# Performance work log

Measured on AMD Instinct MI355X. Metric: run time of the kernel, lower is better.

## Reference

```python
import jax, jax.numpy as jnp
import numpy as np

B, N, T = 2, 207, 864
L = 12           # patch_size
D = 96           # embed_dim
EPS = 1e-8
TAU = 1.0


def setup_inputs() -> dict:
    key = jax.random.key(0)
    k1, k2, k3, k4, k5 = jax.random.split(key, 5)
    return {
        "long_term_history": jax.random.normal(k1, (B, N, 1, T), dtype=jnp.float32),
        "adj_mx": jax.random.uniform(k2, (N, N), dtype=jnp.float32),
        "uniform_noise": jax.random.uniform(k3, (N, N), dtype=jnp.float32),
        "conv_weight": jax.random.normal(k4, (D, N, L), dtype=jnp.float32) * 0.02,
        "conv_bias": jax.random.normal(k5, (D,), dtype=jnp.float32) * 0.02,
        "k": 10,
    }


def _sample_k_neighbor_soft(adj_mx, uniform_noise, k):
    n = adj_mx.shape[0]
    logits = jnp.log(jax.nn.relu(adj_mx) + EPS)
    gumbel = -jnp.log(-jnp.log(uniform_noise + EPS))
    soft = jax.nn.softmax((logits + gumbel) / TAU, axis=1)          # [N, N]
    _, topk_idx = jax.lax.top_k(soft, k)                             # [N, k]
    hard = jnp.zeros_like(soft).at[jnp.arange(n)[:, None], topk_idx].set(1.0)
    return soft * hard                                               # [N, N]


def reference(long_term_history, adj_mx, uniform_noise, conv_weight, conv_bias, k):
    b, n, _, t = long_term_history.shape
    p = t // L
    mask = _sample_k_neighbor_soft(adj_mx, uniform_noise, k)         # [N, N]
    # expanded_history[b,i,j,t] = x[b,i,0,t]; neighbors = mask[i,j] * x[b,i,0,t]
    x = long_term_history[:, :, 0, :]                                # [B, N, T]
    neighbors = mask[None, :, :, None] * x[:, :, None, :]            # [B, N, N, T] (dense blow-up, as in source)
    xp = neighbors.reshape(b, n, n, p, L)                            # split T -> P patches of length L
    # Conv2d(N -> D, kernel (L,1), stride (L,1)) == contraction over (neighbor channel j, in-patch l)
    out = jnp.einsum('bijpl,djl->bidp', xp, conv_weight) + conv_bias[None, None, :, None]
    return out                                                       # [B, N, D, P]
```

## Files before the change

### kernel.cpp

```cpp
#include <hip/hip_runtime.h>
#include <math.h>

#define NN 207
#define BB 2
#define TT 864
#define LL 12
#define DD 96
#define PP 72
#define EPSF 1e-8f

__global__ __launch_bounds__(256) void stpe_fused_kernel(
    const float* __restrict__ x,
    const float* __restrict__ adj,
    const float* __restrict__ noise,
    const float* __restrict__ W,
    const float* __restrict__ bias,
    const int*   __restrict__ kptr,
    float*       __restrict__ out)
{
    __shared__ float s_score[NN];
    __shared__ float s_x[TT];
    __shared__ float s_weff[DD * LL];
    __shared__ float s_topS[32];
    __shared__ int   s_topI[32];
    __shared__ float s_m, s_sum;

    const int blk = blockIdx.x;
    const int b   = blk / NN;
    const int i   = blk - b * NN;
    const int tid = threadIdx.x;
    const int kk  = min(*kptr, 32);

    if (tid < NN) {
        float a = fmaxf(adj[i * NN + tid], 0.0f) + EPSF;
        float u = noise[i * NN + tid] + EPSF;
        float g = -logf(-logf(u));
        s_score[tid] = logf(a) + g;
    }
    for (int t = tid; t < TT; t += 256) s_x[t] = x[(b * NN + i) * TT + t];
    __syncthreads();

    if (tid < 64) {
        const int lane = tid;
        float v[4], orig[4];
        #pragma unroll
        for (int q = 0; q < 4; ++q) {
            int c = lane + 64 * q;
            v[q] = (c < NN) ? s_score[c] : -INFINITY;
            orig[q] = v[q];
        }
        float m = 0.0f;
        for (int it = 0; it < kk; ++it) {
            float bv = v[0]; int bi = lane;
            #pragma unroll
            for (int q = 1; q < 4; ++q)
                if (v[q] > bv) { bv = v[q]; bi = lane + 64 * q; }
            #pragma unroll
            for (int off = 32; off > 0; off >>= 1) {
                float ov = __shfl_xor(bv, off);
                int   oi = __shfl_xor(bi, off);
                if (ov > bv || (ov == bv && oi < bi)) { bv = ov; bi = oi; }
            }
            if (it == 0) m = bv;
            if (lane == 0) { s_topS[it] = bv; s_topI[it] = bi; }
            if ((bi & 63) == lane) v[bi >> 6] = -INFINITY;
        }
        float se = 0.0f;
        #pragma unroll
        for (int q = 0; q < 4; ++q) {
            int c = lane + 64 * q;
            if (c < NN) se += expf(orig[q] - m);
        }
        #pragma unroll
        for (int off = 32; off > 0; off >>= 1) se += __shfl_xor(se, off);
        if (lane == 0) { s_m = m; s_sum = se; }
    }
    __syncthreads();

    if (tid < kk) s_topS[tid] = expf(s_topS[tid] - s_m) / s_sum;
    __syncthreads();

    for (int e = tid; e < DD * LL; e += 256) {
        int d = e / LL, l = e - d * LL;
        float acc = 0.0f;
        for (int t = 0; t < kk; ++t)
            acc += s_topS[t] * W[(d * NN + s_topI[t]) * LL + l];
        s_weff[e] = acc;
    }
    __syncthreads();

    for (int e = tid; e < DD * PP; e += 256) {
        int d = e / PP, p = e - d * PP;
        float acc = bias[d];
        const float* xr = &s_x[p * LL];
        const float* wr = &s_weff[d * LL];
        #pragma unroll
        for (int l = 0; l < LL; ++l) acc += xr[l] * wr[l];
        out[((b * NN + i) * DD + d) * PP + p] = acc;
    }
}

extern "C" void kernel_launch(void* const* d_in, const int* in_sizes, int n_in,
                              void* d_out, int out_size, void* d_ws, size_t ws_size,
                              hipStream_t stream) {
    const float* x     = (const float*)d_in[0];
    const float* adj   = (const float*)d_in[1];
    const float* noise = (const float*)d_in[2];
    const float* W     = (const float*)d_in[3];
    const float* bias  = (const float*)d_in[4];
    const int*   kptr  = (const int*)d_in[5];
    float* out = (float*)d_out;

    stpe_fused_kernel<<<BB * NN, 256, 0, stream>>>(x, adj, noise, W, bias, kptr, out);
}
```

Baseline: 85.44 us.

## Share mask and effective weights across batch; vectorize loads and stores

Each block now handles one node row for both batch elements, so the Gumbel top-k selection and the effective weight gather run once per row instead of once per batch. Global loads of x and W and the output stores use float4, and the softmax normalization is folded into the top-k warp, which removes one barrier. The grid drops to 207 blocks, which may underfill the GPU's compute units and halves parallelism in exchange for removing redundant work.

After: 83.97 us. No clear change (-1.7%).

```diff
diff --git a/kernel.cpp b/kernel.cpp
--- a/kernel.cpp
+++ b/kernel.cpp
@@ -19,25 +19,31 @@
     float*       __restrict__ out)
 {
     __shared__ float s_score[NN];
-    __shared__ float s_x[TT];
+    __shared__ float s_x[BB][TT];
     __shared__ float s_weff[DD * LL];
+    __shared__ float s_bias[DD];
     __shared__ float s_topS[32];
     __shared__ int   s_topI[32];
-    __shared__ float s_m, s_sum;
 
-    const int blk = blockIdx.x;
-    const int b   = blk / NN;
-    const int i   = blk - b * NN;
+    const int i   = blockIdx.x;
     const int tid = threadIdx.x;
     const int kk  = min(*kptr, 32);
 
     if (tid < NN) {
         float a = fmaxf(adj[i * NN + tid], 0.0f) + EPSF;
         float u = noise[i * NN + tid] + EPSF;
-        float g = -logf(-logf(u));
-        s_score[tid] = logf(a) + g;
+        s_score[tid] = logf(a) - logf(-logf(u));
     }
-    for (int t = tid; t < TT; t += 256) s_x[t] = x[(b * NN + i) * TT + t];
+    if (tid < DD) s_bias[tid] = bias[tid];
+
+    {
+        const float4* x4  = (const float4*)x;
+        float4*       sx4 = (float4*)&s_x[0][0];
+        for (int q = tid; q < BB * (TT / 4); q += 256) {
+            int b = q / (TT / 4), r = q - b * (TT / 4);
+            sx4[q] = x4[(b * NN + i) * (TT / 4) + r];
+        }
+    }
     __syncthreads();
 
     if (tid < 64) {
@@ -49,7 +55,7 @@
             v[q] = (c < NN) ? s_score[c] : -INFINITY;
             orig[q] = v[q];
         }
-        float m = 0.0f;
+        float m = 0.0f, myv = 0.0f; int myi = 0;
         for (int it = 0; it < kk; ++it) {
             float bv = v[0]; int bi = lane;
             #pragma unroll
@@ -62,7 +68,7 @@
                 if (ov > bv || (ov == bv && oi < bi)) { bv = ov; bi = oi; }
             }
             if (it == 0) m = bv;
-            if (lane == 0) { s_topS[it] = bv; s_topI[it] = bi; }
+            if (lane == it) { myv = bv; myi = bi; }
             if ((bi & 63) == lane) v[bi >> 6] = -INFINITY;
         }
         float se = 0.0f;
@@ -73,30 +79,52 @@
         }
         #pragma unroll
         for (int off = 32; off > 0; off >>= 1) se += __shfl_xor(se, off);
-        if (lane == 0) { s_m = m; s_sum = se; }
+        if (lane < kk) {
+            s_topS[lane] = expf(myv - m) / se;
+            s_topI[lane] = myi;
+        }
     }
     __syncthreads();
 
-    if (tid < kk) s_topS[tid] = expf(s_topS[tid] - s_m) / s_sum;
-    __syncthreads();
-
-    for (int e = tid; e < DD * LL; e += 256) {
-        int d = e / LL, l = e - d * LL;
-        float acc = 0.0f;
-        for (int t = 0; t < kk; ++t)
-            acc += s_topS[t] * W[(d * NN + s_topI[t]) * LL + l];
-        s_weff[e] = acc;
+    {
+        const float4* W4 = (const float4*)W;
+        float4* weff4 = (float4*)s_weff;
+        for (int e = tid; e < DD * 3; e += 256) {
+            int d = e / 3, c = e - d * 3;
+            float4 acc = {0.f, 0.f, 0.f, 0.f};
+            for (int t = 0; t < kk; ++t) {
+                float s  = s_topS[t];
+                float4 w = W4[(d * NN + s_topI[t]) * 3 + c];
+                acc.x += s * w.x; acc.y += s * w.y;
+                acc.z += s * w.z; acc.w += s * w.w;
+            }
+            weff4[e] = acc;
+        }
     }
     __syncthreads();
 
-    for (int e = tid; e < DD * PP; e += 256) {
-        int d = e / PP, p = e - d * PP;
-        float acc = bias[d];
-        const float* xr = &s_x[p * LL];
-        const float* wr = &s_weff[d * LL];
-        #pragma unroll
-        for (int l = 0; l < LL; ++l) acc += xr[l] * wr[l];
-        out[((b * NN + i) * DD + d) * PP + p] = acc;
+    {
+        float4* out4 = (float4*)out;
+        for (int e = tid; e < BB * DD * (PP / 4); e += 256) {
+            int b = e / (DD * (PP / 4));
+            int r = e - b * (DD * (PP / 4));
+            int d = r / (PP / 4);
+            int c = r - d * (PP / 4);
+            int p0 = c * 4;
+            const float* wr = &s_weff[d * LL];
+            float bd = s_bias[d];
+            float o[4];
+            #pragma unroll
+            for (int q = 0; q < 4; ++q) {
+                const float* xr = &s_x[b][(p0 + q) * LL];
+                float a = bd;
+                #pragma unroll
+                for (int l = 0; l < LL; ++l) a += xr[l] * wr[l];
+                o[q] = a;
+            }
+            float4 val = {o[0], o[1], o[2], o[3]};
+            out4[((b * NN + i) * DD + d) * (PP / 4) + c] = val;
+        }
     }
 }
 
@@ -111,5 +139,5 @@
     const int*   kptr  = (const int*)d_in[5];
     float* out = (float*)d_out;
 
-    stpe_fused_kernel<<<BB * NN, 256, 0, stream>>>(x, adj, noise, W, bias, kptr, out);
+    stpe_fused_kernel<<<NN, 256, 0, stream>>>(x, adj, noise, W, bias, kptr, out);
 }
```
